# Kernel tuning notes

Hardware: AMD Instinct MI355X
Metric: run time of the kernel (lower is better)

The kernel has to match this reference:

```python
import jax, jax.numpy as jnp
import numpy as np

D_HALF = 255
H = 2 * D_HALF + 1   # 511 channels (2*d+1)
L = 2048             # sequence length
N = 32               # S4D complex state modes per channel
NLAYERS = 4          # l
EPS = 1e-5


def setup_inputs() -> dict:
    key = jax.random.key(0)
    ks = jax.random.split(key, 10)
    Z = jax.random.normal(ks[0], (H, L), dtype=jnp.float32)
    # S4D-Lin initialization
    dt_min, dt_max = 1e-3, 1e-1
    log_dt = (jax.random.uniform(ks[1], (H,), dtype=jnp.float32)
              * (np.log(dt_max) - np.log(dt_min)) + np.log(dt_min))
    A_real_log = jnp.log(0.5 * jnp.ones((H, N), dtype=jnp.float32))
    A_imag = jnp.pi * jnp.broadcast_to(jnp.arange(N, dtype=jnp.float32), (H, N))
    C_re = jax.random.normal(ks[2], (H, N), dtype=jnp.float32)
    C_im = jax.random.normal(ks[3], (H, N), dtype=jnp.float32)
    D_skip = jax.random.normal(ks[4], (H,), dtype=jnp.float32)
    glu_w = jax.random.normal(ks[5], (2 * H, H), dtype=jnp.float32) / np.sqrt(H)
    glu_b = jnp.zeros((2 * H,), dtype=jnp.float32)
    ln_g = jnp.ones((H,), dtype=jnp.float32)
    ln_b = jnp.zeros((H,), dtype=jnp.float32)
    return {"Z": Z, "log_dt": log_dt, "A_real_log": A_real_log, "A_imag": A_imag,
            "C_re": C_re, "C_im": C_im, "D_skip": D_skip,
            "glu_w": glu_w, "glu_b": glu_b, "ln_g": ln_g, "ln_b": ln_b}


def _s4d_kernel(log_dt, A_real_log, A_imag, C_re, C_im):
    # A: (H,N) complex with negative real part; ZOH discretization kernel
    A = -jnp.exp(A_real_log) + 1j * A_imag
    dtA = A * jnp.exp(log_dt)[:, None]                  # (H,N)
    Ccoef = (C_re + 1j * C_im) * (jnp.exp(dtA) - 1.0) / A  # (H,N)
    V = jnp.exp(dtA[:, :, None] * jnp.arange(L, dtype=jnp.float32))  # (H,N,L)
    return 2.0 * jnp.einsum('hn,hnl->hl', Ccoef, V).real  # (H,L)


def _s4_block(Z, K, D_skip, glu_w, glu_b):
    # Z: (B,H,L); causal FFT convolution with kernel K (H,L)
    n = 2 * L
    Kf = jnp.fft.rfft(K, n=n)                  # (H, L+1)
    Uf = jnp.fft.rfft(Z, n=n)                  # (B,H,L+1)
    y = jnp.fft.irfft(Uf * Kf, n=n)[..., :L]   # (B,H,L)
    y = y + D_skip[:, None] * Z
    y = jax.nn.gelu(y)
    # output 1x1 conv H -> 2H followed by GLU over channels
    y2 = jnp.einsum('oh,bhl->bol', glu_w, y) + glu_b[:, None]
    return y2[:, :H] * jax.nn.sigmoid(y2[:, H:])


def _layernorm_channels(Z, g, b):
    # LayerNorm over the channel dim (module does norm(Z.transpose(-1,-2)).transpose(-1,-2))
    zt = jnp.swapaxes(Z, -1, -2)               # (B,L,H)
    mu = jnp.mean(zt, axis=-1, keepdims=True)
    var = jnp.mean((zt - mu) ** 2, axis=-1, keepdims=True)
    zt = (zt - mu) * jax.lax.rsqrt(var + EPS) * g + b
    return jnp.swapaxes(zt, -1, -2)


def reference(Z, log_dt, A_real_log, A_imag, C_re, C_im, D_skip, glu_w, glu_b, ln_g, ln_b):
    K = _s4d_kernel(log_dt, A_real_log, A_imag, C_re, C_im)
    z = Z[None]                                # unsqueeze(0) -> (1,H,L)
    for _ in range(NLAYERS):                   # mode='auto': shared layer, l iterations
        residual = z
        z = _s4_block(z, K, D_skip, glu_w, glu_b)
        z = z + residual
        z = _layernorm_channels(z, ln_g, ln_b)
    return z[0]                                # squeeze(0) -> (H,L)
```

## Files before the change

### kernel.cpp

```cpp
#include <hip/hip_runtime.h>
#include <hip/hip_bf16.h>
#include <math.h>

#define H 511
#define L 2048
#define NST 32
#define NLAYERS 4
#define LN_EPS 1e-5f
#define NCH 32
#define TC (L / NCH)
#define HN (H * NST)
#define HP 512
#define GBK 64
#define GBN 64
#define NSTRIPE 16

typedef __attribute__((ext_vector_type(8))) short short8;
typedef __attribute__((ext_vector_type(4))) float f32x4;

__device__ __forceinline__ ushort f2bf(float v) {
    __hip_bfloat16 b = __float2bfloat16(v);
    return *reinterpret_cast<ushort*>(&b);
}

__global__ __launch_bounds__(256) void pre_kernel(
    const float* __restrict__ log_dt,
    const float* __restrict__ A_real_log,
    const float* __restrict__ A_imag,
    const float* __restrict__ C_re,
    const float* __restrict__ C_im,
    const float* __restrict__ W,
    float* __restrict__ wr_o, float* __restrict__ wi_o,
    float* __restrict__ cr_o, float* __restrict__ ci_o,
    ushort* __restrict__ wbf)
{
    int idx = blockIdx.x * blockDim.x + threadIdx.x;
    if (idx < HN) {
        int h = idx / NST;
        float Ar = -expf(A_real_log[idx]);
        float Ai = A_imag[idx];
        float dt = expf(log_dt[h]);
        float dr = Ar * dt, di = Ai * dt;
        float er = expf(dr);
        float wr = er * cosf(di);
        float wi = er * sinf(di);
        float den = Ar * Ar + Ai * Ai;
        float a = wr - 1.0f, b = wi;
        float inv = 1.0f / den;
        float qr = (a * Ar + b * Ai) * inv;
        float qi = (b * Ar - a * Ai) * inv;
        wr_o[idx] = wr; wi_o[idx] = wi;
        cr_o[idx] = 2.0f * (C_re[idx] * qr - C_im[idx] * qi);
        ci_o[idx] = 2.0f * (C_re[idx] * qi + C_im[idx] * qr);
    }
    if (idx < 2 * H * HP) {
        int r = idx / HP, k = idx % HP;
        float v = (k < H) ? W[(size_t)r * H + k] : 0.0f;
        wbf[idx] = f2bf(v);
    }
}

template <int CTRL, int ROW_MASK>
__device__ __forceinline__ float dpp_add(float x) {
    int r = __builtin_amdgcn_update_dpp(0, __float_as_int(x), CTRL, ROW_MASK, 0xf, true);
    return x + __int_as_float(r);
}
__device__ __forceinline__ float reduce32_to_lane31(float p) {
    p = dpp_add<0x111, 0xf>(p);
    p = dpp_add<0x112, 0xf>(p);
    p = dpp_add<0x114, 0xf>(p);
    p = dpp_add<0x118, 0xf>(p);
    p = dpp_add<0x142, 0xa>(p);
    return p;
}

__device__ __forceinline__ float gelu_tanh(float v) {
    const float c0 = 0.7978845608028654f;
    float t = tanhf(c0 * (v + 0.044715f * v * v * v));
    return 0.5f * v * (1.0f + t);
}

__global__ __launch_bounds__(1024) void conv_fused(
    const float* __restrict__ z,
    const float* __restrict__ wr_,
    const float* __restrict__ wi_,
    const float* __restrict__ cr_,
    const float* __restrict__ ci_,
    const float* __restrict__ D_skip,
    ushort* __restrict__ yb)
{
    __shared__ float zs[L];
    __shared__ float ber[NCH][NST];
    __shared__ float bei[NCH][NST];
    __shared__ float ysf[L];

    const int tid  = threadIdx.x;
    const int wv   = tid >> 6;
    const int half = (tid >> 5) & 1;
    const int ln   = tid & 31;
    const int c    = wv * 2 + half;
    const int h    = blockIdx.x;

    *(float2*)&zs[tid * 2] = *(const float2*)&z[(size_t)h * L + tid * 2];

    const int cidx = h * NST + ln;
    const float wr = wr_[cidx], wi = wi_[cidx];
    const float cr = cr_[cidx], ci = ci_[cidx];
    const float Dh = D_skip[h];
    __syncthreads();

    float sr = 0.f, si = 0.f;
    {
        const float* zp = &zs[c * TC];
        #pragma unroll 4
        for (int l = 0; l < TC; ++l) {
            float zl = zp[l];
            float nsr = fmaf(wr, sr, fmaf(-wi, si, zl));
            float nsi = fmaf(wr, si, wi * sr);
            sr = nsr; si = nsi;
        }
    }
    ber[c][ln] = sr;
    bei[c][ln] = si;
    __syncthreads();

    if (tid < 32) {
        float wtr = wr, wti = wi;
        #pragma unroll
        for (int k = 0; k < 6; ++k) {
            float nr = wtr * wtr - wti * wti;
            float ni = 2.0f * wtr * wti;
            wtr = nr; wti = ni;
        }
        float er = 0.f, ei = 0.f;
        #pragma unroll
        for (int cc = 0; cc < NCH; ++cc) {
            float s_r = ber[cc][tid], s_i = bei[cc][tid];
            ber[cc][tid] = er; bei[cc][tid] = ei;
            float ner = fmaf(wtr, er, fmaf(-wti, ei, s_r));
            float nei = fmaf(wtr, ei, fmaf(wti, er, s_i));
            er = ner; ei = nei;
        }
    }
    __syncthreads();

    sr = ber[c][ln];
    si = bei[c][ln];
    {
        const float* zp = &zs[c * TC];
        float* yp = &ysf[c * TC];
        for (int l = 0; l < TC; ++l) {
            float zl = zp[l];
            float nsr = fmaf(wr, sr, fmaf(-wi, si, zl));
            float nsi = fmaf(wr, si, wi * sr);
            sr = nsr; si = nsi;
            float p = fmaf(cr, sr, -ci * si);
            p = reduce32_to_lane31(p);
            if (ln == 31) yp[l] = fmaf(Dh, zl, p);
        }
    }
    __syncthreads();

    {
        ushort2 v;
        v.x = f2bf(gelu_tanh(ysf[tid * 2]));
        v.y = f2bf(gelu_tanh(ysf[tid * 2 + 1]));
        *(ushort2*)&yb[(size_t)h * L + tid * 2] = v;
    }
}

__global__ __launch_bounds__(256) void glu_mfma(
    const ushort* __restrict__ wbf,
    const ushort* __restrict__ yb,
    const float* __restrict__ bias,
    const float* __restrict__ zres,
    float* __restrict__ out,
    float* __restrict__ psum,
    float* __restrict__ psq)
{
    __shared__ ushort As1[32 * GBK];
    __shared__ ushort As2[32 * GBK];
    __shared__ ushort Bs[GBN * GBK];
    __shared__ ushort tempT[4][32 * 40];
    __shared__ float  sls[2][64];
    __shared__ float  slq[2][64];

    const int tid = threadIdx.x;
    const int h0 = blockIdx.y * 32;
    const int l0 = blockIdx.x * GBN;
    const int wid = tid >> 6;
    const int lane = tid & 63;
    const int wrow = (wid >> 1) * 16;
    const int wcol = (wid & 1) * 32;

    f32x4 acc1[2] = {{0.f,0.f,0.f,0.f},{0.f,0.f,0.f,0.f}};
    f32x4 acc2[2] = {{0.f,0.f,0.f,0.f},{0.f,0.f,0.f,0.f}};

    const int ar = tid >> 3;
    const int ak = tid & 7;
    const int hq1 = (h0 + ar < H) ? (h0 + ar) : (H - 1);
    const int hq2 = hq1 + H;
    const int aswz = ak ^ (ar & 7);

    const int tm   = tid >> 6;
    const int t64  = tid & 63;
    const int ksub = (tm & 1) * 32;
    const int lsub = (tm >> 1) * 32;
    const int bkl  = t64 >> 1;
    const int bhalf= t64 & 1;
    const int blr  = t64 >> 1;
    const int bkh  = t64 & 1;

    for (int k0 = 0; k0 < HP; k0 += GBK) {
        {
            short8 va1 = *(const short8*)&wbf[(size_t)hq1 * HP + k0 + ak * 8];
            short8 va2 = *(const short8*)&wbf[(size_t)hq2 * HP + k0 + ak * 8];
            *(short8*)&As1[ar * GBK + aswz * 8] = va1;
            *(short8*)&As2[ar * GBK + aswz * 8] = va2;
        }
        {
            const int kg = k0 + ksub + bkl;
            short8 v0 = {0,0,0,0,0,0,0,0}, v1 = {0,0,0,0,0,0,0,0};
            if (kg < H) {
                const ushort* row = &yb[(size_t)kg * L + l0 + lsub + bhalf * 16];
                v0 = *(const short8*)&row[0];
                v1 = *(const short8*)&row[8];
            }
            ushort* tp = &tempT[tm][0];
            #pragma unroll
            for (int j = 0; j < 8; ++j)
                tp[(bhalf * 16 + j) * 40 + bkl] = (ushort)v0[j];
            #pragma unroll
            for (int j = 0; j < 8; ++j)
                tp[(bhalf * 16 + 8 + j) * 40 + bkl] = (ushort)v1[j];
        }
        __syncthreads();
        {
            const ushort* tp = &tempT[tm][0];
            short8 b0 = *(const short8*)&tp[blr * 40 + bkh * 16];
            short8 b1 = *(const short8*)&tp[blr * 40 + bkh * 16 + 8];
            const int L_ = lsub + blr;
            const int kg0 = (ksub >> 3) + bkh * 2;
            *(short8*)&Bs[L_ * GBK + ((kg0    ) ^ (L_ & 7)) * 8] = b0;
            *(short8*)&Bs[L_ * GBK + ((kg0 + 1) ^ (L_ & 7)) * 8] = b1;
        }
        __syncthreads();

        #pragma unroll
        for (int kk = 0; kk < 2; ++kk) {
            const int arow = wrow + (lane & 15);
            const int kg = kk * 4 + (lane >> 4);
            short8 a1 = *(const short8*)&As1[arow * GBK + (kg ^ (arow & 7)) * 8];
            short8 a2 = *(const short8*)&As2[arow * GBK + (kg ^ (arow & 7)) * 8];
            #pragma unroll
            for (int nf = 0; nf < 2; ++nf) {
                const int brow = wcol + nf * 16 + (lane & 15);
                short8 b = *(const short8*)&Bs[brow * GBK + (kg ^ (brow & 7)) * 8];
                acc1[nf] = __builtin_amdgcn_mfma_f32_16x16x32_bf16(a1, b, acc1[nf], 0, 0, 0);
                acc2[nf] = __builtin_amdgcn_mfma_f32_16x16x32_bf16(a2, b, acc2[nf], 0, 0, 0);
            }
        }
        __syncthreads();
    }

    float ps[2] = {0.f, 0.f}, pq[2] = {0.f, 0.f};
    #pragma unroll
    for (int nf = 0; nf < 2; ++nf) {
        const int col = l0 + wcol + nf * 16 + (lane & 15);
        #pragma unroll
        for (int r = 0; r < 4; ++r) {
            const int h = h0 + wrow + (lane >> 4) * 4 + r;
            if (h < H) {
                float v1 = acc1[nf][r] + bias[h];
                float v2 = acc2[nf][r] + bias[h + H];
                float o = v1 * (1.0f / (1.0f + expf(-v2))) + zres[(size_t)h * L + col];
                out[(size_t)h * L + col] = o;
                ps[nf] += o;
                pq[nf] = fmaf(o, o, pq[nf]);
            }
        }
    }
    #pragma unroll
    for (int nf = 0; nf < 2; ++nf) {
        ps[nf] += __shfl_xor(ps[nf], 16, 64);
        ps[nf] += __shfl_xor(ps[nf], 32, 64);
        pq[nf] += __shfl_xor(pq[nf], 16, 64);
        pq[nf] += __shfl_xor(pq[nf], 32, 64);
        if ((lane >> 4) == 0) {
            int cl = wcol + nf * 16 + lane;
            sls[wid >> 1][cl] = ps[nf];
            slq[wid >> 1][cl] = pq[nf];
        }
    }
    __syncthreads();
    if (tid < 64) {
        psum[(size_t)blockIdx.y * L + l0 + tid] = sls[0][tid] + sls[1][tid];
        psq [(size_t)blockIdx.y * L + l0 + tid] = slq[0][tid] + slq[1][tid];
    }
}

__global__ __launch_bounds__(256) void ln_apply(
    const float* __restrict__ zpre,
    const float* __restrict__ psum, const float* __restrict__ psq,
    const float* __restrict__ g, const float* __restrict__ b,
    float* __restrict__ out)
{
    const int tx = threadIdx.x & 63;
    const int ty = threadIdx.x >> 6;
    const int l = blockIdx.x * 64 + tx;
    const int s = blockIdx.y;

    float S = 0.f, Q = 0.f;
    #pragma unroll
    for (int k = 0; k < NSTRIPE; ++k) {
        S += psum[(size_t)k * L + l];
        Q += psq[(size_t)k * L + l];
    }
    const float invH = 1.0f / (float)H;
    float mu = S * invH;
    float var = Q * invH - mu * mu;
    float rstd = rsqrtf(var + LN_EPS);

    const int hbase = s * 32;
    #pragma unroll
    for (int j = 0; j < 8; ++j) {
        int h = hbase + ty + j * 4;
        if (h < H) {
            float v = zpre[(size_t)h * L + l];
            out[(size_t)h * L + l] = (v - mu) * rstd * g[h] + b[h];
        }
    }
}

extern "C" void kernel_launch(void* const* d_in, const int* in_sizes, int n_in,
                              void* d_out, int out_size, void* d_ws, size_t ws_size,
                              hipStream_t stream) {
    const float* Z          = (const float*)d_in[0];
    const float* log_dt     = (const float*)d_in[1];
    const float* A_real_log = (const float*)d_in[2];
    const float* A_imag     = (const float*)d_in[3];
    const float* C_re       = (const float*)d_in[4];
    const float* C_im       = (const float*)d_in[5];
    const float* D_skip     = (const float*)d_in[6];
    const float* glu_w      = (const float*)d_in[7];
    const float* glu_b      = (const float*)d_in[8];
    const float* ln_g       = (const float*)d_in[9];
    const float* ln_b       = (const float*)d_in[10];

    float* out = (float*)d_out;
    float* ws  = (float*)d_ws;

    float* wr   = ws;
    float* wi   = wr + HN;
    float* cr   = wi + HN;
    float* ci   = cr + HN;
    float* zbuf = ci + HN;
    float* psum = zbuf + (size_t)H * L;
    float* psq  = psum + (size_t)NSTRIPE * L;
    ushort* yb  = (ushort*)(psq + (size_t)NSTRIPE * L);
    ushort* wbf = yb + (size_t)H * L;

    pre_kernel<<<(2 * H * HP + 255) / 256, 256, 0, stream>>>(
        log_dt, A_real_log, A_imag, C_re, C_im, glu_w,
        wr, wi, cr, ci, wbf);

    const dim3 gg(L / GBN, (H + 31) / 32);
    const dim3 lg(L / 64, NSTRIPE);

    for (int layer = 0; layer < NLAYERS; ++layer) {
        const float* zcur = (layer == 0) ? Z : zbuf;

        conv_fused<<<H, 1024, 0, stream>>>(
            zcur, wr, wi, cr, ci, D_skip, yb);
        glu_mfma<<<gg, 256, 0, stream>>>(wbf, yb, glu_b, zcur, out, psum, psq);

        float* lnout = (layer < NLAYERS - 1) ? zbuf : out;
        ln_apply<<<lg, 256, 0, stream>>>(out, psum, psq, ln_g, ln_b, lnout);
    }
}
```

Before: 222.6 us.

## Fuse LayerNorm apply into next layer's conv and GLU kernels

The standalone LayerNorm pass that ran between layers is removed. Each layer's conv and GLU kernels now rebuild the mean and rstd from the previous layer's stripe partial sums and normalize their input on the fly, so the 'out' buffer serves as both the pre-norm input and the output. The partial-sum buffers are double-buffered so the previous layer's stats stay intact while the current layer writes new ones, and only the final layer still runs a separate LN pass. This saves three launches and one full read/write of the activation per layer, in exchange for repeated small reads of the 16-stripe stats in every conv and GLU block.

Result: slower. 238.7 us (+7.2%).

```diff
diff --git a/kernel.cpp b/kernel.cpp
--- a/kernel.cpp
+++ b/kernel.cpp
@@ -81,7 +81,12 @@
 }
 
 __global__ __launch_bounds__(1024) void conv_fused(
-    const float* __restrict__ z,
+    const float* __restrict__ zsrc,
+    const float* __restrict__ psum_p,
+    const float* __restrict__ psq_p,
+    const float* __restrict__ lng,
+    const float* __restrict__ lnb,
+    const int donorm,
     const float* __restrict__ wr_,
     const float* __restrict__ wi_,
     const float* __restrict__ cr_,
@@ -101,7 +106,28 @@
     const int c    = wv * 2 + half;
     const int h    = blockIdx.x;
 
-    *(float2*)&zs[tid * 2] = *(const float2*)&z[(size_t)h * L + tid * 2];
+    {
+        const int c0 = tid * 2;
+        float2 v = *(const float2*)&zsrc[(size_t)h * L + c0];
+        if (donorm) {
+            float2 S = {0.f, 0.f}, Q = {0.f, 0.f};
+            #pragma unroll
+            for (int k = 0; k < NSTRIPE; ++k) {
+                float2 sv = *(const float2*)&psum_p[(size_t)k * L + c0];
+                float2 qv = *(const float2*)&psq_p[(size_t)k * L + c0];
+                S.x += sv.x; S.y += sv.y;
+                Q.x += qv.x; Q.y += qv.y;
+            }
+            const float invH = 1.0f / (float)H;
+            float mu0 = S.x * invH, mu1 = S.y * invH;
+            float rs0 = rsqrtf(Q.x * invH - mu0 * mu0 + LN_EPS);
+            float rs1 = rsqrtf(Q.y * invH - mu1 * mu1 + LN_EPS);
+            float gh = lng[h], bh = lnb[h];
+            v.x = (v.x - mu0) * rs0 * gh + bh;
+            v.y = (v.y - mu1) * rs1 * gh + bh;
+        }
+        *(float2*)&zs[tid * 2] = v;
+    }
 
     const int cidx = h * NST + ln;
     const float wr = wr_[cidx], wi = wi_[cidx];
@@ -174,9 +200,14 @@
     const ushort* __restrict__ yb,
     const float* __restrict__ bias,
     const float* __restrict__ zres,
+    const float* __restrict__ psum_p,
+    const float* __restrict__ psq_p,
+    const float* __restrict__ lng,
+    const float* __restrict__ lnb,
+    const int donorm,
     float* __restrict__ out,
-    float* __restrict__ psum,
-    float* __restrict__ psq)
+    float* __restrict__ psum_c,
+    float* __restrict__ psq_c)
 {
     __shared__ ushort As1[32 * GBK];
     __shared__ ushort As2[32 * GBK];
@@ -267,13 +298,27 @@
     #pragma unroll
     for (int nf = 0; nf < 2; ++nf) {
         const int col = l0 + wcol + nf * 16 + (lane & 15);
+        float mu = 0.f, rs = 1.f;
+        if (donorm) {
+            float S = 0.f, Q = 0.f;
+            #pragma unroll
+            for (int k = 0; k < NSTRIPE; ++k) {
+                S += psum_p[(size_t)k * L + col];
+                Q += psq_p[(size_t)k * L + col];
+            }
+            const float invH = 1.0f / (float)H;
+            mu = S * invH;
+            rs = rsqrtf(Q * invH - mu * mu + LN_EPS);
+        }
         #pragma unroll
         for (int r = 0; r < 4; ++r) {
             const int h = h0 + wrow + (lane >> 4) * 4 + r;
             if (h < H) {
+                float zv = zres[(size_t)h * L + col];
+                if (donorm) zv = (zv - mu) * rs * lng[h] + lnb[h];
                 float v1 = acc1[nf][r] + bias[h];
                 float v2 = acc2[nf][r] + bias[h + H];
-                float o = v1 * (1.0f / (1.0f + expf(-v2))) + zres[(size_t)h * L + col];
+                float o = v1 * (1.0f / (1.0f + expf(-v2))) + zv;
                 out[(size_t)h * L + col] = o;
                 ps[nf] += o;
                 pq[nf] = fmaf(o, o, pq[nf]);
@@ -294,13 +339,12 @@
     }
     __syncthreads();
     if (tid < 64) {
-        psum[(size_t)blockIdx.y * L + l0 + tid] = sls[0][tid] + sls[1][tid];
-        psq [(size_t)blockIdx.y * L + l0 + tid] = slq[0][tid] + slq[1][tid];
+        psum_c[(size_t)blockIdx.y * L + l0 + tid] = sls[0][tid] + sls[1][tid];
+        psq_c [(size_t)blockIdx.y * L + l0 + tid] = slq[0][tid] + slq[1][tid];
     }
 }
 
 __global__ __launch_bounds__(256) void ln_apply(
-    const float* __restrict__ zpre,
     const float* __restrict__ psum, const float* __restrict__ psq,
     const float* __restrict__ g, const float* __restrict__ b,
     float* __restrict__ out)
@@ -326,7 +370,7 @@
     for (int j = 0; j < 8; ++j) {
         int h = hbase + ty + j * 4;
         if (h < H) {
-            float v = zpre[(size_t)h * L + l];
+            float v = out[(size_t)h * L + l];
             out[(size_t)h * L + l] = (v - mu) * rstd * g[h] + b[h];
         }
     }
@@ -350,14 +394,15 @@
     float* out = (float*)d_out;
     float* ws  = (float*)d_ws;
 
-    float* wr   = ws;
-    float* wi   = wr + HN;
-    float* cr   = wi + HN;
-    float* ci   = cr + HN;
-    float* zbuf = ci + HN;
-    float* psum = zbuf + (size_t)H * L;
-    float* psq  = psum + (size_t)NSTRIPE * L;
-    ushort* yb  = (ushort*)(psq + (size_t)NSTRIPE * L);
+    float* wr    = ws;
+    float* wi    = wr + HN;
+    float* cr    = wi + HN;
+    float* ci    = cr + HN;
+    float* psumA = ci + HN;
+    float* psqA  = psumA + (size_t)NSTRIPE * L;
+    float* psumB = psqA + (size_t)NSTRIPE * L;
+    float* psqB  = psumB + (size_t)NSTRIPE * L;
+    ushort* yb  = (ushort*)(psqB + (size_t)NSTRIPE * L);
     ushort* wbf = yb + (size_t)H * L;
 
     pre_kernel<<<(2 * H * HP + 255) / 256, 256, 0, stream>>>(
@@ -368,13 +413,19 @@
     const dim3 lg(L / 64, NSTRIPE);
 
     for (int layer = 0; layer < NLAYERS; ++layer) {
-        const float* zcur = (layer == 0) ? Z : zbuf;
+        const int donorm = (layer > 0);
+        const float* zsrc = (layer == 0) ? Z : out;
+        float* psum_c = (layer & 1) ? psumB : psumA;
+        float* psq_c  = (layer & 1) ? psqB  : psqA;
+        const float* psum_p = (layer & 1) ? psumA : psumB;
+        const float* psq_p  = (layer & 1) ? psqA  : psqB;
 
         conv_fused<<<H, 1024, 0, stream>>>(
-            zcur, wr, wi, cr, ci, D_skip, yb);
-        glu_mfma<<<gg, 256, 0, stream>>>(wbf, yb, glu_b, zcur, out, psum, psq);
-
-        float* lnout = (layer < NLAYERS - 1) ? zbuf : out;
-        ln_apply<<<lg, 256, 0, stream>>>(out, psum, psq, ln_g, ln_b, lnout);
-    }
-}
+            zsrc, psum_p, psq_p, ln_g, ln_b, donorm,
+            wr, wi, cr, ci, D_skip, yb);
+        glu_mfma<<<gg, 256, 0, stream>>>(
+            wbf, yb, glu_b, zsrc, psum_p, psq_p, ln_g, ln_b, donorm,
+            out, psum_c, psq_c);
+    }
+    ln_apply<<<lg, 256, 0, stream>>>(psumB, psqB, ln_g, ln_b, out);
+}
```

## Parallelize chunk carry propagation with warp-level scan and precompute w^64

Applied to the files above, without the earlier changes.

Replaces the serial 32-step carry propagation across chunks, which ran on a single 32-lane group, with a Kogge-Stone shuffle scan in which all 1024 threads each handle one (chunk, state) pair. The per-state chunk multiplier w^64 is now computed once in the precompute kernel instead of on every launch. Unroll factors are raised for the scan loops and the launch bounds are tightened. This removes a serial bottleneck where most of the block sat idle, at the cost of extra workspace and possible register pressure.

Measured after the change: 232.2 us. 1.04x slower.

```diff
diff --git a/kernel.cpp b/kernel.cpp
--- a/kernel.cpp
+++ b/kernel.cpp
@@ -32,6 +32,7 @@
     const float* __restrict__ W,
     float* __restrict__ wr_o, float* __restrict__ wi_o,
     float* __restrict__ cr_o, float* __restrict__ ci_o,
+    float* __restrict__ w64r_o, float* __restrict__ w64i_o,
     ushort* __restrict__ wbf)
 {
     int idx = blockIdx.x * blockDim.x + threadIdx.x;
@@ -52,6 +53,14 @@
         wr_o[idx] = wr; wi_o[idx] = wi;
         cr_o[idx] = 2.0f * (C_re[idx] * qr - C_im[idx] * qi);
         ci_o[idx] = 2.0f * (C_re[idx] * qi + C_im[idx] * qr);
+        float sr = wr, si = wi;
+        #pragma unroll
+        for (int k = 0; k < 6; ++k) {
+            float nr = sr * sr - si * si;
+            float ni = 2.0f * sr * si;
+            sr = nr; si = ni;
+        }
+        w64r_o[idx] = sr; w64i_o[idx] = si;
     }
     if (idx < 2 * H * HP) {
         int r = idx / HP, k = idx % HP;
@@ -80,12 +89,14 @@
     return 0.5f * v * (1.0f + t);
 }
 
-__global__ __launch_bounds__(1024) void conv_fused(
+__global__ __launch_bounds__(1024, 8) void conv_fused(
     const float* __restrict__ z,
     const float* __restrict__ wr_,
     const float* __restrict__ wi_,
     const float* __restrict__ cr_,
     const float* __restrict__ ci_,
+    const float* __restrict__ w64r_,
+    const float* __restrict__ w64i_,
     const float* __restrict__ D_skip,
     ushort* __restrict__ yb)
 {
@@ -112,7 +123,7 @@
     float sr = 0.f, si = 0.f;
     {
         const float* zp = &zs[c * TC];
-        #pragma unroll 4
+        #pragma unroll 8
         for (int l = 0; l < TC; ++l) {
             float zl = zp[l];
             float nsr = fmaf(wr, sr, fmaf(-wi, si, zl));
@@ -124,23 +135,30 @@
     bei[c][ln] = si;
     __syncthreads();
 
-    if (tid < 32) {
-        float wtr = wr, wti = wi;
+    {
+        const int lam = tid & 63;
+        const int c2 = lam & 31;
+        const int n2 = ((tid >> 6) << 1) | (lam >> 5);
+        float Ir = ber[c2][n2], Ii = bei[c2][n2];
+        float Wr = w64r_[h * NST + n2], Wi = w64i_[h * NST + n2];
         #pragma unroll
-        for (int k = 0; k < 6; ++k) {
-            float nr = wtr * wtr - wti * wti;
-            float ni = 2.0f * wtr * wti;
-            wtr = nr; wti = ni;
-        }
-        float er = 0.f, ei = 0.f;
-        #pragma unroll
-        for (int cc = 0; cc < NCH; ++cc) {
-            float s_r = ber[cc][tid], s_i = bei[cc][tid];
-            ber[cc][tid] = er; bei[cc][tid] = ei;
-            float ner = fmaf(wtr, er, fmaf(-wti, ei, s_r));
-            float nei = fmaf(wtr, ei, fmaf(wti, er, s_i));
-            er = ner; ei = nei;
-        }
+        for (int d = 1; d < 32; d <<= 1) {
+            float pr = __shfl_up(Ir, d, 32);
+            float pi = __shfl_up(Ii, d, 32);
+            if (c2 < d) { pr = 0.f; pi = 0.f; }
+            float tr = fmaf(Wr, pr, -Wi * pi);
+            float ti = fmaf(Wr, pi,  Wi * pr);
+            Ir += tr; Ii += ti;
+            float nWr = Wr * Wr - Wi * Wi;
+            float nWi = 2.0f * Wr * Wi;
+            Wr = nWr; Wi = nWi;
+        }
+        float Cr = __shfl_up(Ir, 1, 32);
+        float Ci = __shfl_up(Ii, 1, 32);
+        if (c2 == 0) { Cr = 0.f; Ci = 0.f; }
+        __syncthreads();
+        ber[c2][n2] = Cr;
+        bei[c2][n2] = Ci;
     }
     __syncthreads();
 
@@ -149,6 +167,7 @@
     {
         const float* zp = &zs[c * TC];
         float* yp = &ysf[c * TC];
+        #pragma unroll 4
         for (int l = 0; l < TC; ++l) {
             float zl = zp[l];
             float nsr = fmaf(wr, sr, fmaf(-wi, si, zl));
@@ -350,19 +369,21 @@
     float* out = (float*)d_out;
     float* ws  = (float*)d_ws;
 
-    float* wr   = ws;
-    float* wi   = wr + HN;
-    float* cr   = wi + HN;
-    float* ci   = cr + HN;
-    float* zbuf = ci + HN;
-    float* psum = zbuf + (size_t)H * L;
-    float* psq  = psum + (size_t)NSTRIPE * L;
+    float* wr    = ws;
+    float* wi    = wr + HN;
+    float* cr    = wi + HN;
+    float* ci    = cr + HN;
+    float* w64r  = ci + HN;
+    float* w64i  = w64r + HN;
+    float* zbuf  = w64i + HN;
+    float* psum  = zbuf + (size_t)H * L;
+    float* psq   = psum + (size_t)NSTRIPE * L;
     ushort* yb  = (ushort*)(psq + (size_t)NSTRIPE * L);
     ushort* wbf = yb + (size_t)H * L;
 
     pre_kernel<<<(2 * H * HP + 255) / 256, 256, 0, stream>>>(
         log_dt, A_real_log, A_imag, C_re, C_im, glu_w,
-        wr, wi, cr, ci, wbf);
+        wr, wi, cr, ci, w64r, w64i, wbf);
 
     const dim3 gg(L / GBN, (H + 31) / 32);
     const dim3 lg(L / 64, NSTRIPE);
@@ -371,7 +392,7 @@
         const float* zcur = (layer == 0) ? Z : zbuf;
 
         conv_fused<<<H, 1024, 0, stream>>>(
-            zcur, wr, wi, cr, ci, D_skip, yb);
+            zcur, wr, wi, cr, ci, w64r, w64i, D_skip, yb);
         glu_mfma<<<gg, 256, 0, stream>>>(wbf, yb, glu_b, zcur, out, psum, psq);
 
         float* lnout = (layer < NLAYERS - 1) ? zbuf : out;
```
